# Optimization experiments

Measured on AMD Instinct MI355X. Metric: run time of the kernel, lower is better.

The kernel has to match this reference:

```python
import jax, jax.numpy as jnp
import numpy as np

B, S, N, E = 16, 2048, 256, 4096      # batch, tokens, max entities, edges per sample
H, LD, ETR = 512, 16, 768             # hidden_size, label_emb_dim, transformer dim
D = H + LD                            # graph_dim = 528
C1 = 3                                # num_edge_classes + 1
GL = 2                                # gcn_layers
NLBL = 15                             # num_node_classes + 2


def setup_inputs() -> dict:
    key = jax.random.key(0)
    ks = jax.random.split(key, 14)
    s = 0.02
    inp = {}
    inp["emb"] = jax.random.normal(ks[0], (B, S, ETR), jnp.float32)
    inp["ent_indices"] = jax.random.randint(ks[1], (B, S), 0, N + 1)
    inp["ent_labels"] = jax.random.randint(ks[2], (B, N), 0, NLBL)
    inp["edge_index"] = jax.random.randint(ks[3], (B, 2, E), 0, N + 1)
    inp["edge_attr"] = jax.random.randint(ks[4], (B, E), 0, C1)
    inp["cands"] = jax.random.randint(ks[5], (B, N + 1, N + 1), 0, 2).astype(bool)
    inp["W_red"] = jax.random.normal(ks[6], (ETR, H), jnp.float32) * s
    inp["b_red"] = jnp.zeros((H,), jnp.float32)
    inp["emb_label_tbl"] = jax.random.normal(ks[7], (NLBL, LD), jnp.float32) * s
    inp["W_gcn"] = jax.random.normal(ks[8], (C1, GL, D, D), jnp.float32) * s
    inp["b_gcn"] = jnp.zeros((C1, GL, D), jnp.float32)
    inp["W_head"] = jax.random.normal(ks[9], (D, D), jnp.float32) * s
    inp["b_head"] = jnp.zeros((D,), jnp.float32)
    inp["W_tail"] = jax.random.normal(ks[10], (D, D), jnp.float32) * s
    inp["b_tail"] = jnp.zeros((D,), jnp.float32)
    inp["W_out"] = jax.random.normal(ks[11], (D, C1), jnp.float32) * s
    inp["b_out"] = jnp.zeros((C1,), jnp.float32)
    return inp


def _gcn_layer(x, src, dst, w_e, W, b):
    """PyG GCNConv with edge weights w_e (0/1 relation mask) and self loops.
    x: [n, D]; src/dst: [E]; aggregation flow source->target."""
    n = x.shape[0]
    h = x @ W
    deg = jax.ops.segment_sum(w_e, dst, num_segments=n) + 1.0  # +1 self loop
    dinv = jax.lax.rsqrt(deg)
    coef = w_e * dinv[src] * dinv[dst]                         # D^-1/2 A D^-1/2
    agg = jax.ops.segment_sum(coef[:, None] * h[src], dst, num_segments=n)
    return agg + h / deg[:, None] + b                          # self-loop norm = 1/deg


def reference(emb, ent_indices, ent_labels, edge_index, edge_attr, cands,
              W_red, b_red, emb_label_tbl, W_gcn, b_gcn,
              W_head, b_head, W_tail, b_tail, W_out, b_out):
    n_nodes = cands.shape[1]  # max_num_ent + 1
    # fc_reduction of frozen transformer embeddings
    red = emb @ W_red + b_red                                   # [B,S,H]
    # tag-based segment aggregation: max over (mask * emb) == max(segment_max, 0)
    seg_max = jax.vmap(lambda e, ids: jax.ops.segment_max(e, ids, num_segments=n_nodes))(red, ent_indices)
    ent_hidden = jnp.maximum(seg_max, 0.0).at[:, 0, :].set(0.0)  # tag 0 stays zero
    # label embeddings: tag t uses ent_labels[:, t-1]; zeroed where label==0
    lab = emb_label_tbl[ent_labels] * (ent_labels != 0)[..., None].astype(red.dtype)
    lab0 = jnp.broadcast_to(emb_label_tbl[0], (lab.shape[0], 1, lab.shape[-1]))
    label_part = jnp.concatenate([lab0, lab], axis=1)           # [B,n_nodes,LD]
    x0 = jnp.concatenate([label_part, ent_hidden], axis=-1)     # [B,n_nodes,D]
    # multi-relation GCN: per edge class, stacked GCNConv, summed then averaged
    src, dst = edge_index[:, 0], edge_index[:, 1]
    layer_v = jax.vmap(_gcn_layer, in_axes=(0, 0, 0, 0, None, None))
    result = jnp.zeros_like(x0)
    n_cls = W_gcn.shape[0]
    for c in range(n_cls):
        w_e = (edge_attr == c).astype(x0.dtype)
        x = x0
        for l in range(W_gcn.shape[1]):
            x = layer_v(x, src, dst, w_e, W_gcn[c, l], b_gcn[c, l])
        result = result + x
    result = result / n_cls
    # head/tail projections and 'add' pairwise features gated by candidate mask
    x_head = result @ W_head + b_head
    x_tail = result @ W_tail + b_tail
    m = cands[:, :, 1:].astype(x0.dtype)                        # [B,n_nodes,n_nodes-1]
    # fc_out is linear: ((h_i + t_j) * m_ij) @ W + b == m_ij*(hW_i + tW_j) + b
    hW = x_head @ W_out                                         # [B,n_nodes,C1]
    tW = x_tail[:, 1:] @ W_out                                  # [B,n_nodes-1,C1]
    logits = (hW[:, :, None, :] + tW[:, None, :, :]) * m[..., None] + b_out
    return logits  # [B, n_nodes, n_nodes-1, C1] edge-class logits
```

## Files before the change

### kernel.cpp

```cpp
#include <hip/hip_runtime.h>
#include <hip/hip_bf16.h>

typedef unsigned short u16;
typedef __attribute__((ext_vector_type(8))) short short8;
typedef __attribute__((ext_vector_type(4))) float floatx4;

#define B_ 16
#define S_ 2048
#define NNODE 257
#define E_ 4096
#define ETR_ 768
#define H_ 512
#define D_ 528
#define KPAD 544
#define NC 3
#define NROW (B_*NNODE)
#define DD (D_*D_)

#define BM 128
#define BN 128
#define BK 32

__device__ inline u16 f2b(float x) {
    __hip_bfloat16 h = __float2bfloat16(x);
    return *(u16*)&h;
}

__device__ inline void gll16(const u16* g, u16* l) {
    __builtin_amdgcn_global_load_lds(
        (const __attribute__((address_space(1))) void*)g,
        (__attribute__((address_space(3))) void*)l,
        16, 0, 0);
}

__device__ inline int clampi(int v, int hi) { return v < hi ? v : hi; }

__global__ void cvt_bf16(const float* __restrict__ in, u16* __restrict__ out, int n4)
{
    const int i = blockIdx.x * 256 + threadIdx.x;
    if (i < n4) {
        const float4 f = ((const float4*)in)[i];
        ushort4 o;
        o.x = f2b(f.x); o.y = f2b(f.y); o.z = f2b(f.z); o.w = f2b(f.w);
        ((ushort4*)out)[i] = o;
    }
}

__global__ void transpose_cvt(const float* __restrict__ in, u16* __restrict__ out,
                              int R, int Cc, size_t instride, size_t outstride,
                              int opitch)
{
    __shared__ float t[32][33];
    const int z = blockIdx.z;
    const int tx = threadIdx.x & 31, ty = threadIdx.x >> 5;
    const int c0 = blockIdx.x * 32, r0 = blockIdx.y * 32;
    const float* ip = in + z * instride;
    u16* op = out + z * outstride;
#pragma unroll
    for (int i = 0; i < 4; i++) {
        const int r = r0 + ty + i * 8, c = c0 + tx;
        if (r < R && c < Cc) t[ty + i * 8][tx] = ip[(size_t)r * Cc + c];
    }
    __syncthreads();
#pragma unroll
    for (int i = 0; i < 4; i++) {
        const int c = c0 + ty + i * 8, r = r0 + tx;
        if (c < Cc && r < R) op[(size_t)c * opitch + r] = f2b(t[tx][ty + i * 8]);
    }
}

template<int SWZ, int OB16>
__global__ __launch_bounds__(256)
void gemm_mfma(const u16* __restrict__ A, const u16* __restrict__ Wt,
               void* __restrict__ Cv, int M, int N, int K, float scale,
               size_t astride, size_t wstride, size_t cstride)
{
    __shared__ u16 SS[8192];
    const int tid = threadIdx.x;
    const int wave = tid >> 6, lane = tid & 63;
    const int quad = lane >> 4, l16 = lane & 15;
    const int z = blockIdx.z;
    int bx = blockIdx.x, by = blockIdx.y;
    if (SWZ) {
        const int lin = blockIdx.x + (blockIdx.y << 2);
        bx = (lin >> 3) & 3;
        by = (lin & 7) + ((lin >> 5) << 3);
    }
    const int m0 = by * BM, n0 = bx * BN;

    floatx4 acc[2][8];
#pragma unroll
    for (int t = 0; t < 2; t++)
#pragma unroll
        for (int u = 0; u < 8; u++)
#pragma unroll
            for (int r = 0; r < 4; r++) acc[t][u][r] = 0.f;

    const int srow = tid >> 2;
    const int scol = (tid & 3) * 8;
    const u16* aP0 = A + z * astride + (size_t)clampi(m0 + srow,      M - 1) * K + scol;
    const u16* aP1 = A + z * astride + (size_t)clampi(m0 + 64 + srow, M - 1) * K + scol;
    const u16* bP0 = Wt + z * wstride + (size_t)clampi(n0 + srow,      N - 1) * K + scol;
    const u16* bP1 = Wt + z * wstride + (size_t)clampi(n0 + 64 + srow, N - 1) * K + scol;
    u16* const ls = &SS[0] + wave * 512;

    for (int k0 = 0; k0 < K; k0 += BK) {
        gll16(aP0 + k0, ls);
        gll16(aP1 + k0, ls + 2048);
        gll16(bP0 + k0, ls + 4096);
        gll16(bP1 + k0, ls + 6144);
        __syncthreads();
        short8 af[2], bfv[8];
        af[0] = *(const short8*)&SS[(wave * 32 + l16) * 32 + quad * 8];
        af[1] = *(const short8*)&SS[(wave * 32 + 16 + l16) * 32 + quad * 8];
#pragma unroll
        for (int u = 0; u < 8; u++)
            bfv[u] = *(const short8*)&SS[4096 + (u * 16 + l16) * 32 + quad * 8];
#pragma unroll
        for (int t = 0; t < 2; t++)
#pragma unroll
            for (int u = 0; u < 8; u++)
                acc[t][u] = __builtin_amdgcn_mfma_f32_16x16x32_bf16(af[t], bfv[u], acc[t][u], 0, 0, 0);
        __syncthreads();
    }

#pragma unroll
    for (int t = 0; t < 2; t++) {
#pragma unroll
        for (int r = 0; r < 4; r++) {
            const int m = m0 + wave * 32 + t * 16 + quad * 4 + r;
            if (m >= M) continue;
#pragma unroll
            for (int u = 0; u < 8; u++) {
                const int n = n0 + u * 16 + l16;
                if (n < N) {
                    if (OB16) {
                        u16* Cb = (u16*)Cv;
                        Cb[z * cstride + (size_t)m * N + n] = f2b(acc[t][u][r] * scale);
                    } else {
                        float* Cf = (float*)Cv;
                        Cf[z * cstride + (size_t)m * N + n] = acc[t][u][r] * scale;
                    }
                }
            }
        }
    }
}

template<int MODE>
__global__ __launch_bounds__(256)
void gemm64(const float* __restrict__ A, const float* __restrict__ W,
            const float* __restrict__ bias, float* __restrict__ C,
            int M, int N, int K, float scale,
            const int* __restrict__ segidx, float* __restrict__ segout)
{
    __shared__ float Asl[16][68];
    __shared__ float Bsl[16][64];
    const int tid = threadIdx.x;
    const int tx = tid & 15, ty = tid >> 4;
    const int m0 = blockIdx.y * 64, n0 = blockIdx.x * 64;
    const int arow = tid >> 2, acol = (tid & 3) * 4;
    const int brow = tid >> 4, bcol = (tid & 15) * 4;

    float acc[4][4];
#pragma unroll
    for (int i = 0; i < 4; i++)
#pragma unroll
        for (int j = 0; j < 4; j++) acc[i][j] = 0.f;

    for (int kk = 0; kk < K; kk += 16) {
        float4 av = make_float4(0.f, 0.f, 0.f, 0.f);
        if (m0 + arow < M) av = *(const float4*)(A + (size_t)(m0 + arow) * K + kk + acol);
        Asl[acol + 0][arow] = av.x; Asl[acol + 1][arow] = av.y;
        Asl[acol + 2][arow] = av.z; Asl[acol + 3][arow] = av.w;
        float4 bv = make_float4(0.f, 0.f, 0.f, 0.f);
        if (n0 + bcol < N) bv = *(const float4*)(W + (size_t)(kk + brow) * N + n0 + bcol);
        *(float4*)&Bsl[brow][bcol] = bv;
        __syncthreads();
#pragma unroll
        for (int k = 0; k < 16; k++) {
            const float4 a = *(const float4*)&Asl[k][ty * 4];
            const float4 b = *(const float4*)&Bsl[k][tx * 4];
            const float af[4] = { a.x, a.y, a.z, a.w };
            const float bfv[4] = { b.x, b.y, b.z, b.w };
#pragma unroll
            for (int i = 0; i < 4; i++)
#pragma unroll
                for (int j = 0; j < 4; j++) acc[i][j] += af[i] * bfv[j];
        }
        __syncthreads();
    }

#pragma unroll
    for (int i = 0; i < 4; i++) {
        const int m = m0 + ty * 4 + i;
        if (m >= M) continue;
        if (MODE == 1) {
            const int bb = m >> 11;
            const int idx = segidx[m];
            float* const srow = segout + (((size_t)bb * NNODE + idx) << 9);
#pragma unroll
            for (int j = 0; j < 4; j++) {
                const int n = n0 + tx * 4 + j;
                const float v = acc[i][j] + (bias ? bias[n] : 0.f);
                atomicMax(((int*)srow) + n, __float_as_int(v));
            }
        } else {
#pragma unroll
            for (int j = 0; j < 4; j++) {
                const int n = n0 + tx * 4 + j;
                if (n < N) {
                    const float v = acc[i][j] * scale + (bias ? bias[n] : 0.f);
                    C[(size_t)m * N + n] = v;
                }
            }
        }
    }
}

__global__ void rows_csr(const int* __restrict__ ent_indices,
                         int* __restrict__ rptr, int* __restrict__ rlist)
{
    __shared__ int cnt[NNODE];
    const int b = blockIdx.x;
    const int tid = threadIdx.x;
    const int* idx = ent_indices + (size_t)b * S_;
    for (int i = tid; i < NNODE; i += 256) cnt[i] = 0;
    __syncthreads();
    for (int r = tid; r < S_; r += 256) atomicAdd(&cnt[idx[r]], 1);
    __syncthreads();
    if (tid == 0) {
        int run = 0;
        for (int i = 0; i < NNODE; i++) { const int c = cnt[i]; cnt[i] = run; run += c; }
    }
    __syncthreads();
    for (int i = tid; i < NNODE; i += 256) rptr[b * (NNODE + 1) + i] = cnt[i];
    if (tid == 0) rptr[b * (NNODE + 1) + NNODE] = S_;
    __syncthreads();
    for (int r = tid; r < S_; r += 256) {
        const int pos = atomicAdd(&cnt[idx[r]], 1);
        rlist[(size_t)b * S_ + pos] = r;
    }
}

__global__ __launch_bounds__(256)
void segmax_x0(const u16* __restrict__ redC, const int* __restrict__ rptr,
               const int* __restrict__ rlist, const float* __restrict__ b_red,
               const int* __restrict__ ent_labels, const float* __restrict__ tbl,
               u16* __restrict__ x0b)
{
    const int bn = blockIdx.x;
    const int b = bn / NNODE, n = bn % NNODE;
    const int tid = threadIdx.x;
    const int c0 = tid * 2;
    const int start = rptr[b * (NNODE + 1) + n];
    const int end   = (n == 0) ? start : rptr[b * (NNODE + 1) + n + 1];
    float m0 = -INFINITY, m1 = -INFINITY;
    const int* rl = rlist + (size_t)b * S_;
    for (int i = start; i < end; i++) {
        const u16* row = redC + ((size_t)b * S_ + rl[i]) * H_;
        const unsigned v = *(const unsigned*)(row + c0);
        m0 = fmaxf(m0, __uint_as_float((v & 0xffffu) << 16));
        m1 = fmaxf(m1, __uint_as_float(v & 0xffff0000u));
    }
    float h0, h1;
    if (n == 0) { h0 = 0.f; h1 = 0.f; }
    else {
        h0 = fmaxf(m0 + b_red[c0], 0.f);
        h1 = fmaxf(m1 + b_red[c0 + 1], 0.f);
    }
    u16* orow = x0b + (size_t)bn * KPAD;
    *(unsigned*)(orow + 16 + c0) = (unsigned)f2b(h0) | ((unsigned)f2b(h1) << 16);
    if (tid < 16) {
        float v;
        if (n == 0) v = tbl[tid];
        else {
            const int lab = ent_labels[b * (NNODE - 1) + (n - 1)];
            v = (lab != 0) ? tbl[lab * 16 + tid] : 0.f;
        }
        orow[tid] = f2b(v);
    } else if (tid < 32) {
        orow[512 + tid] = 0;
    }
}

template<int OUTB>
__global__ void build_x0(const float* __restrict__ seg, const int* __restrict__ ent_labels,
                         const float* __restrict__ tbl, float* __restrict__ x0f,
                         u16* __restrict__ x0b)
{
    const int bn = blockIdx.x;
    const int b = bn / NNODE, n = bn % NNODE;
    const int CMAX = OUTB ? KPAD : D_;
    for (int col = threadIdx.x; col < CMAX; col += blockDim.x) {
        float v;
        if (col >= D_) {
            v = 0.f;
        } else if (col < 16) {
            if (n == 0) v = tbl[col];
            else {
                const int lab = ent_labels[b * (NNODE - 1) + (n - 1)];
                v = (lab != 0) ? tbl[lab * 16 + col] : 0.f;
            }
        } else {
            v = (n == 0) ? 0.f : seg[(((size_t)b * NNODE + n) << 9) + (col - 16)];
        }
        if (OUTB) x0b[(size_t)bn * KPAD + col] = f2b(v);
        else      x0f[(size_t)bn * D_ + col] = v;
    }
}

__global__ void csr_build(const int* __restrict__ edge_index, const int* __restrict__ edge_attr,
                          float* __restrict__ degf, int* __restrict__ csr_ptr,
                          int2* __restrict__ csr_sc)
{
    __shared__ int cnt[NC * NNODE];
    __shared__ float dinvl[NC * NNODE];
    const int b = blockIdx.x;
    const int tid = threadIdx.x;
    const int* src = edge_index + (size_t)b * 2 * E_;
    const int* dst = src + E_;
    const int* attr = edge_attr + (size_t)b * E_;

    for (int i = tid; i < NC * NNODE; i += 256) cnt[i] = 0;
    __syncthreads();
    for (int e = tid; e < E_; e += 256) atomicAdd(&cnt[attr[e] * NNODE + dst[e]], 1);
    __syncthreads();
    for (int i = tid; i < NC * NNODE; i += 256) {
        const float d = (float)cnt[i] + 1.0f;
        degf[(size_t)b * NC * NNODE + i] = d;
        dinvl[i] = rsqrtf(d);
    }
    __syncthreads();
    if (tid == 0) {
        int run = 0;
        for (int i = 0; i < NC * NNODE; i++) { const int c = cnt[i]; cnt[i] = run; run += c; }
    }
    __syncthreads();
    for (int i = tid; i < NC * NNODE; i += 256) csr_ptr[(size_t)b * NC * NNODE + i] = cnt[i];
    __syncthreads();
    for (int e = tid; e < E_; e += 256) {
        const int a = attr[e], d = dst[e], s = src[e];
        const int pos = atomicAdd(&cnt[a * NNODE + d], 1);
        const float cf = dinvl[a * NNODE + s] * dinvl[a * NNODE + d];
        csr_sc[(size_t)b * E_ + pos] = make_int2(s, __float_as_int(cf));
    }
}

template<int OUT>
__global__ __launch_bounds__(256)
void gcn_gather(const float* __restrict__ h, size_t hstride,
                const float* __restrict__ degf,
                const int* __restrict__ csr_ptr, const int2* __restrict__ csr_sc,
                const float* __restrict__ bias_base, size_t bias_stride,
                float* __restrict__ outf, u16* __restrict__ outb, size_t ostride,
                int cls0)
{
    const int bn = blockIdx.x;
    const int cls = cls0 + blockIdx.y;
    const int b = bn / NNODE, n = bn % NNODE;
    const int tid = threadIdx.x;
    const int base = b * NC * NNODE + cls * NNODE + n;
    const float d = degf[base];
    const int start = csr_ptr[base];
    const int cnt = (int)d - 1;
    const float inv = 1.0f / d;
    const float* hp = h + blockIdx.y * hstride;
    const float* bias = bias_base + cls * bias_stride;
    const float* hrow = hp + (size_t)bn * D_;
    const int c0 = tid, c1 = tid + 256, c2 = tid + 512;
    float a0 = hrow[c0] * inv + bias[c0];
    float a1 = hrow[c1] * inv + bias[c1];
    float a2 = (c2 < D_) ? hrow[c2] * inv + bias[c2] : 0.f;
    const int2* scp = csr_sc + (size_t)b * E_ + start;
    int2 sc = (cnt > 0) ? scp[0] : make_int2(0, 0);
    for (int i = 0; i < cnt; i++) {
        const int2 cur = sc;
        if (i + 1 < cnt) sc = scp[i + 1];
        const float cf = __int_as_float(cur.y);
        const float* hs = hp + ((size_t)b * NNODE + cur.x) * D_;
        a0 += cf * hs[c0];
        a1 += cf * hs[c1];
        if (c2 < D_) a2 += cf * hs[c2];
    }
    if (OUT == 0) {
        u16* orow = outb + blockIdx.y * ostride + (size_t)bn * KPAD;
        orow[c0] = f2b(a0); orow[c1] = f2b(a1); if (c2 < D_) orow[c2] = f2b(a2);
        if (tid >= 16 && tid < 32) orow[512 + tid] = 0;
    } else if (OUT == 1) {
        float* orow = outf + (size_t)bn * D_;
        orow[c0] += a0; orow[c1] += a1; if (c2 < D_) orow[c2] += a2;
    } else if (OUT == 2) {
        float* orow = outf + blockIdx.y * ostride + (size_t)bn * D_;
        orow[c0] = a0; orow[c1] = a1; if (c2 < D_) orow[c2] = a2;
    } else {
        float* orow = outf + (size_t)bn * D_;
        atomicAdd(&orow[c0], a0); atomicAdd(&orow[c1], a1);
        if (c2 < D_) atomicAdd(&orow[c2], a2);
    }
}

__global__ void rowdot3(const float* __restrict__ x, const float* __restrict__ w,
                        float* __restrict__ out)
{
    const int row = blockIdx.x;
    const int lane = threadIdx.x;
    float a0 = 0.f, a1 = 0.f, a2 = 0.f;
    for (int d = lane; d < D_; d += 64) {
        const float xv = x[(size_t)row * D_ + d];
        a0 += xv * w[d * 3 + 0];
        a1 += xv * w[d * 3 + 1];
        a2 += xv * w[d * 3 + 2];
    }
#pragma unroll
    for (int off = 32; off > 0; off >>= 1) {
        a0 += __shfl_down(a0, off, 64);
        a1 += __shfl_down(a1, off, 64);
        a2 += __shfl_down(a2, off, 64);
    }
    if (lane == 0) {
        out[(size_t)row * 3 + 0] = a0;
        out[(size_t)row * 3 + 1] = a1;
        out[(size_t)row * 3 + 2] = a2;
    }
}

__global__ void prep_heads(const float* __restrict__ W_head, const float* __restrict__ W_tail,
                           const float* __restrict__ b_head, const float* __restrict__ b_tail,
                           const float* __restrict__ W_out,
                           float* __restrict__ Whw, float* __restrict__ Wtw,
                           float* __restrict__ bias6)
{
    const int r = blockIdx.x;
    const int lane = threadIdx.x;
    const float* x; float* o;
    if (r < D_)            { x = W_head + (size_t)r * D_;        o = Whw + (size_t)r * 3; }
    else if (r < 2 * D_)   { x = W_tail + (size_t)(r - D_) * D_; o = Wtw + (size_t)(r - D_) * 3; }
    else if (r == 2 * D_)  { x = b_head;                         o = bias6; }
    else                   { x = b_tail;                         o = bias6 + 3; }
    float a0 = 0.f, a1 = 0.f, a2 = 0.f;
    for (int d = lane; d < D_; d += 64) {
        const float xv = x[d];
        a0 += xv * W_out[d * 3 + 0];
        a1 += xv * W_out[d * 3 + 1];
        a2 += xv * W_out[d * 3 + 2];
    }
#pragma unroll
    for (int off = 32; off > 0; off >>= 1) {
        a0 += __shfl_down(a0, off, 64);
        a1 += __shfl_down(a1, off, 64);
        a2 += __shfl_down(a2, off, 64);
    }
    if (lane == 0) { o[0] = a0; o[1] = a1; o[2] = a2; }
}

__global__ __launch_bounds__(256)
void rowdot6(const float* __restrict__ x3, size_t zstride,
             const float* __restrict__ Whw, const float* __restrict__ Wtw,
             const float* __restrict__ bias6,
             float* __restrict__ hw, float* __restrict__ tw)
{
    const int row = blockIdx.x * 4 + (threadIdx.x >> 6);
    const int lane = threadIdx.x & 63;
    const float* p0 = x3 + (size_t)row * D_;
    const float* p1 = p0 + zstride;
    const float* p2 = p1 + zstride;
    float h0 = 0.f, h1 = 0.f, h2 = 0.f, t0 = 0.f, t1 = 0.f, t2 = 0.f;
    for (int d = lane; d < D_; d += 64) {
        const float xv = (p0[d] + p1[d] + p2[d]) * (1.f / 3.f);
        h0 += xv * Whw[d * 3 + 0]; h1 += xv * Whw[d * 3 + 1]; h2 += xv * Whw[d * 3 + 2];
        t0 += xv * Wtw[d * 3 + 0]; t1 += xv * Wtw[d * 3 + 1]; t2 += xv * Wtw[d * 3 + 2];
    }
#pragma unroll
    for (int off = 32; off > 0; off >>= 1) {
        h0 += __shfl_down(h0, off, 64); h1 += __shfl_down(h1, off, 64); h2 += __shfl_down(h2, off, 64);
        t0 += __shfl_down(t0, off, 64); t1 += __shfl_down(t1, off, 64); t2 += __shfl_down(t2, off, 64);
    }
    if (lane == 0) {
        hw[(size_t)row * 3 + 0] = h0 + bias6[0];
        hw[(size_t)row * 3 + 1] = h1 + bias6[1];
        hw[(size_t)row * 3 + 2] = h2 + bias6[2];
        tw[(size_t)row * 3 + 0] = t0 + bias6[3];
        tw[(size_t)row * 3 + 1] = t1 + bias6[4];
        tw[(size_t)row * 3 + 2] = t2 + bias6[5];
    }
}

__global__ __launch_bounds__(256)
void final_logits(const float* __restrict__ hw, const float* __restrict__ tw,
                  const int* __restrict__ cands, const float* __restrict__ b_out,
                  float* __restrict__ out)
{
    const int bi = blockIdx.x;
    const int b = bi / NNODE;
    const int j = threadIdx.x;
    const float h0 = hw[bi * 3 + 0], h1 = hw[bi * 3 + 1], h2 = hw[bi * 3 + 2];
    const int tj = b * NNODE + 1 + j;
    const float t0 = tw[tj * 3 + 0], t1 = tw[tj * 3 + 1], t2 = tw[tj * 3 + 2];
    const float m = (cands[(size_t)bi * NNODE + 1 + j] != 0) ? 1.f : 0.f;
    const float bo0 = b_out[0], bo1 = b_out[1], bo2 = b_out[2];
    const size_t o = ((size_t)bi * 256 + j) * 3;
    out[o + 0] = (h0 + t0) * m + bo0;
    out[o + 1] = (h1 + t1) * m + bo1;
    out[o + 2] = (h2 + t2) * m + bo2;
}

extern "C" void kernel_launch(void* const* d_in, const int* in_sizes, int n_in,
                              void* d_out, int out_size, void* d_ws, size_t ws_size,
                              hipStream_t stream)
{
    const float* emb       = (const float*)d_in[0];
    const int* ent_indices = (const int*)d_in[1];
    const int* ent_labels  = (const int*)d_in[2];
    const int* edge_index  = (const int*)d_in[3];
    const int* edge_attr   = (const int*)d_in[4];
    const int* cands       = (const int*)d_in[5];
    const float* W_red     = (const float*)d_in[6];
    const float* b_red     = (const float*)d_in[7];
    const float* tbl       = (const float*)d_in[8];
    const float* W_gcn     = (const float*)d_in[9];
    const float* b_gcn     = (const float*)d_in[10];
    const float* W_head    = (const float*)d_in[11];
    const float* b_head    = (const float*)d_in[12];
    const float* W_tail    = (const float*)d_in[13];
    const float* b_tail    = (const float*)d_in[14];
    const float* W_out     = (const float*)d_in[15];
    const float* b_out     = (const float*)d_in[16];

    char* ws = (char*)d_ws;
    size_t off = 0;
    auto alloc = [&](size_t nbytes) -> char* {
        char* p = ws + off; off = (off + nbytes + 255) & ~(size_t)255; return p;
    };
    const size_t ROWB  = (size_t)NROW * D_ * sizeof(float);
    const size_t RD    = (size_t)NROW * D_;
    const size_t RD2   = (size_t)NROW * KPAD;
    const size_t WGZ   = (size_t)2 * D_ * KPAD;

    char* R0      = alloc((size_t)B_ * S_ * ETR_ * sizeof(u16));
    u16*  emb_bf  = (u16*)R0;
    float* hbuf   = (float*)R0;
    u16*  x1b     = (u16*)(R0 + 3 * ROWB);
    char* R1      = alloc((size_t)B_ * S_ * H_ * sizeof(u16));
    u16*  redC    = (u16*)R1;
    float* result3 = (float*)R1;
    int*  rptr    = (int*)alloc((size_t)B_ * (NNODE + 1) * 4);
    int*  rlist   = (int*)alloc((size_t)B_ * S_ * 4);
    u16*  x0b     = (u16*)alloc((size_t)NROW * KPAD * sizeof(u16));
    u16*  wredT   = (u16*)alloc((size_t)H_ * ETR_ * sizeof(u16));
    u16*  wgcnT   = (u16*)alloc((size_t)NC * WGZ * sizeof(u16));
    float* Whw    = (float*)alloc((size_t)D_ * 3 * 4);
    float* Wtw    = (float*)alloc((size_t)D_ * 3 * 4);
    float* bias6  = (float*)alloc(6 * 4);
    float* degf   = (float*)alloc((size_t)B_ * NC * NNODE * 4);
    float* hwp    = (float*)alloc((size_t)NROW * 3 * 4);
    float* twp    = (float*)alloc((size_t)NROW * 3 * 4);
    int* csr_ptr  = (int*)alloc((size_t)B_ * NC * NNODE * 4);
    int2* csr_sc  = (int2*)alloc((size_t)B_ * E_ * 8);
    const bool fast = (ws_size >= off);

    if (fast) {
        const int n4e = (B_ * S_ * ETR_) / 4;
        cvt_bf16<<<(n4e + 255) / 256, 256, 0, stream>>>(emb, emb_bf, n4e);
        transpose_cvt<<<dim3(16, 24, 1), 256, 0, stream>>>(W_red, wredT, ETR_, H_, 0, 0, ETR_);
        hipMemsetAsync(wgcnT, 0, (size_t)NC * WGZ * sizeof(u16), stream);
        transpose_cvt<<<dim3(17, 17, 6), 256, 0, stream>>>(W_gcn, wgcnT, D_, D_, DD, (size_t)D_ * KPAD, KPAD);

        prep_heads<<<2 * D_ + 2, 64, 0, stream>>>(W_head, W_tail, b_head, b_tail, W_out,
                                                  Whw, Wtw, bias6);

        rows_csr<<<B_, 256, 0, stream>>>(ent_indices, rptr, rlist);

        gemm_mfma<1, 1><<<dim3(H_ / BN, (B_ * S_) / BM, 1), 256, 0, stream>>>(
            emb_bf, wredT, redC, B_ * S_, H_, ETR_, 1.f, 0, 0, 0);
        segmax_x0<<<B_ * NNODE, 256, 0, stream>>>(redC, rptr, rlist, b_red,
                                                  ent_labels, tbl, x0b);

        csr_build<<<B_, 256, 0, stream>>>(edge_index, edge_attr, degf, csr_ptr, csr_sc);

        dim3 gmm((D_ + BN - 1) / BN, (NROW + BM - 1) / BM, NC);
        gemm_mfma<0, 0><<<gmm, 256, 0, stream>>>(
            x0b, wgcnT, hbuf, NROW, D_, KPAD, 1.f, 0, WGZ, RD);
        gcn_gather<0><<<dim3(NROW, NC), 256, 0, stream>>>(
            hbuf, RD, degf, csr_ptr, csr_sc, b_gcn, (size_t)2 * D_,
            nullptr, x1b, RD2, 0);
        gemm_mfma<0, 0><<<gmm, 256, 0, stream>>>(
            x1b, wgcnT + (size_t)D_ * KPAD, hbuf, NROW, D_, KPAD, 1.f, RD2, WGZ, RD);
        gcn_gather<2><<<dim3(NROW, NC), 256, 0, stream>>>(
            hbuf, RD, degf, csr_ptr, csr_sc, b_gcn + D_, (size_t)2 * D_,
            result3, nullptr, RD, 0);

        rowdot6<<<NROW / 4, 256, 0, stream>>>(result3, RD, Whw, Wtw, bias6, hwp, twp);
        final_logits<<<NROW, 256, 0, stream>>>(hwp, twp, cands, b_out, (float*)d_out);
        return;
    }

    off = 0;
    float* bufA = (float*)alloc(ROWB);
    float* bufB = (float*)alloc(ROWB);
    float* bufC = (float*)alloc(ROWB);
    float* bufD = (float*)alloc(ROWB);
    degf = (float*)alloc((size_t)B_ * NC * NNODE * 4);
    hwp  = (float*)alloc((size_t)NROW * 3 * 4);
    twp  = (float*)alloc((size_t)NROW * 3 * 4);
    csr_ptr = (int*)alloc((size_t)B_ * NC * NNODE * 4);
    csr_sc  = (int2*)alloc((size_t)B_ * E_ * 8);

    hipMemsetAsync(bufA, 0, (size_t)B_ * NNODE * H_ * 4, stream);
    hipMemsetAsync(bufD, 0, ROWB, stream);
    gemm64<1><<<dim3(H_ / 64, (B_ * S_) / 64), 256, 0, stream>>>(
        emb, W_red, b_red, nullptr, B_ * S_, H_, ETR_, 1.f, ent_indices, bufA);
    build_x0<0><<<NROW, 256, 0, stream>>>(bufA, ent_labels, tbl, bufB, nullptr);
    csr_build<<<B_, 256, 0, stream>>>(edge_index, edge_attr, degf, csr_ptr, csr_sc);
    dim3 gridG((D_ + 63) / 64, (NROW + 63) / 64);
    for (int c = 0; c < NC; c++) {
        gemm64<0><<<gridG, 256, 0, stream>>>(bufB, W_gcn + (size_t)(c * 2 + 0) * DD,
            nullptr, bufA, NROW, D_, D_, 1.f, nullptr, nullptr);
        gcn_gather<2><<<dim3(NROW, 1), 256, 0, stream>>>(bufA, 0, degf, csr_ptr, csr_sc,
            b_gcn, (size_t)2 * D_, bufC, nullptr, 0, c);
        gemm64<0><<<gridG, 256, 0, stream>>>(bufC, W_gcn + (size_t)(c * 2 + 1) * DD,
            nullptr, bufA, NROW, D_, D_, 1.f, nullptr, nullptr);
        gcn_gather<1><<<dim3(NROW, 1), 256, 0, stream>>>(bufA, 0, degf, csr_ptr, csr_sc,
            b_gcn + D_, (size_t)2 * D_, bufD, nullptr, 0, c);
    }
    gemm64<0><<<gridG, 256, 0, stream>>>(bufD, W_head, b_head, bufB,
        NROW, D_, D_, 1.f / 3.f, nullptr, nullptr);
    gemm64<0><<<gridG, 256, 0, stream>>>(bufD, W_tail, b_tail, bufC,
        NROW, D_, D_, 1.f / 3.f, nullptr, nullptr);
    rowdot3<<<NROW, 64, 0, stream>>>(bufB, W_out, hwp);
    rowdot3<<<NROW, 64, 0, stream>>>(bufC, W_out, twp);
    final_logits<<<NROW, 256, 0, stream>>>(hwp, twp, cands, b_out, (float*)d_out);
}
```

Before: 413.7 us.

## Aggregate before GCN matmul, fuse bias, and convert fp32 activations inside GEMM

The GCN layers are reordered as aggregate-then-transform (A·X then W), and the bias add moves into the GEMM epilogue. The separate emb fp32-to-bf16 conversion pass is dropped; the GEMM now loads fp32 A tiles and converts them to bf16 in registers before writing to LDS. The goal is to remove a full-size conversion kernel and one intermediate round trip. In exchange, aggregation gathers bf16 inputs and writes an fp32 buffer that the GEMM then reads. The A-tile loads lose the async global-to-LDS path and double the bytes read for A. Aggregating bf16-rounded layer-1 outputs also changes numerics slightly.

```diff
diff --git a/kernel.cpp b/kernel.cpp
--- a/kernel.cpp
+++ b/kernel.cpp
@@ -25,6 +25,9 @@
     __hip_bfloat16 h = __float2bfloat16(x);
     return *(u16*)&h;
 }
+__device__ inline float b2f(u16 u) {
+    return __uint_as_float(((unsigned)u) << 16);
+}
 
 __device__ inline void gll16(const u16* g, u16* l) {
     __builtin_amdgcn_global_load_lds(
@@ -34,17 +37,6 @@
 }
 
 __device__ inline int clampi(int v, int hi) { return v < hi ? v : hi; }
-
-__global__ void cvt_bf16(const float* __restrict__ in, u16* __restrict__ out, int n4)
-{
-    const int i = blockIdx.x * 256 + threadIdx.x;
-    if (i < n4) {
-        const float4 f = ((const float4*)in)[i];
-        ushort4 o;
-        o.x = f2b(f.x); o.y = f2b(f.y); o.z = f2b(f.z); o.w = f2b(f.w);
-        ((ushort4*)out)[i] = o;
-    }
-}
 
 __global__ void transpose_cvt(const float* __restrict__ in, u16* __restrict__ out,
                               int R, int Cc, size_t instride, size_t outstride,
@@ -71,9 +63,10 @@
 
 template<int SWZ, int OB16>
 __global__ __launch_bounds__(256)
-void gemm_mfma(const u16* __restrict__ A, const u16* __restrict__ Wt,
+void gemm_mfma(const float* __restrict__ A, const u16* __restrict__ Wt,
+               const float* __restrict__ bias_base, size_t bias_stride,
                void* __restrict__ Cv, int M, int N, int K, float scale,
-               size_t astride, size_t wstride, size_t cstride)
+               size_t astride, size_t wstride, size_t cstride, int cpitch)
 {
     __shared__ u16 SS[8192];
     const int tid = threadIdx.x;
@@ -98,17 +91,32 @@
 
     const int srow = tid >> 2;
     const int scol = (tid & 3) * 8;
-    const u16* aP0 = A + z * astride + (size_t)clampi(m0 + srow,      M - 1) * K + scol;
-    const u16* aP1 = A + z * astride + (size_t)clampi(m0 + 64 + srow, M - 1) * K + scol;
+    const float* aF0 = A + z * astride + (size_t)clampi(m0 + srow,      M - 1) * K + scol;
+    const float* aF1 = A + z * astride + (size_t)clampi(m0 + 64 + srow, M - 1) * K + scol;
     const u16* bP0 = Wt + z * wstride + (size_t)clampi(n0 + srow,      N - 1) * K + scol;
     const u16* bP1 = Wt + z * wstride + (size_t)clampi(n0 + 64 + srow, N - 1) * K + scol;
     u16* const ls = &SS[0] + wave * 512;
+    u16* const aw0 = &SS[srow * 32 + scol];
+    u16* const aw1 = &SS[2048 + srow * 32 + scol];
 
     for (int k0 = 0; k0 < K; k0 += BK) {
-        gll16(aP0 + k0, ls);
-        gll16(aP1 + k0, ls + 2048);
+        const float4 v0 = *(const float4*)(aF0 + k0);
+        const float4 v1 = *(const float4*)(aF0 + k0 + 4);
+        const float4 v2 = *(const float4*)(aF1 + k0);
+        const float4 v3 = *(const float4*)(aF1 + k0 + 4);
         gll16(bP0 + k0, ls + 4096);
         gll16(bP1 + k0, ls + 6144);
+        short8 p0, p1;
+        p0[0] = (short)f2b(v0.x); p0[1] = (short)f2b(v0.y);
+        p0[2] = (short)f2b(v0.z); p0[3] = (short)f2b(v0.w);
+        p0[4] = (short)f2b(v1.x); p0[5] = (short)f2b(v1.y);
+        p0[6] = (short)f2b(v1.z); p0[7] = (short)f2b(v1.w);
+        p1[0] = (short)f2b(v2.x); p1[1] = (short)f2b(v2.y);
+        p1[2] = (short)f2b(v2.z); p1[3] = (short)f2b(v2.w);
+        p1[4] = (short)f2b(v3.x); p1[5] = (short)f2b(v3.y);
+        p1[6] = (short)f2b(v3.z); p1[7] = (short)f2b(v3.w);
+        *(short8*)aw0 = p0;
+        *(short8*)aw1 = p1;
         __syncthreads();
         short8 af[2], bfv[8];
         af[0] = *(const short8*)&SS[(wave * 32 + l16) * 32 + quad * 8];
@@ -124,6 +132,7 @@
         __syncthreads();
     }
 
+    const float* bias = bias_base ? (bias_base + z * bias_stride) : nullptr;
 #pragma unroll
     for (int t = 0; t < 2; t++) {
 #pragma unroll
@@ -134,12 +143,13 @@
             for (int u = 0; u < 8; u++) {
                 const int n = n0 + u * 16 + l16;
                 if (n < N) {
+                    const float v = acc[t][u][r] * scale + (bias ? bias[n] : 0.f);
                     if (OB16) {
                         u16* Cb = (u16*)Cv;
-                        Cb[z * cstride + (size_t)m * N + n] = f2b(acc[t][u][r] * scale);
+                        Cb[z * cstride + (size_t)m * cpitch + n] = f2b(v);
                     } else {
                         float* Cf = (float*)Cv;
-                        Cf[z * cstride + (size_t)m * N + n] = acc[t][u][r] * scale;
+                        Cf[z * cstride + (size_t)m * cpitch + n] = v;
                     }
                 }
             }
@@ -347,6 +357,43 @@
     }
 }
 
+__global__ __launch_bounds__(256)
+void gcn_agg(const u16* __restrict__ x, size_t xzstride,
+             const float* __restrict__ degf,
+             const int* __restrict__ csr_ptr, const int2* __restrict__ csr_sc,
+             float* __restrict__ y)
+{
+    const int bn = blockIdx.x;
+    const int cls = blockIdx.y;
+    const int b = bn / NNODE, n = bn % NNODE;
+    const int tid = threadIdx.x;
+    const int base = b * NC * NNODE + cls * NNODE + n;
+    const float d = degf[base];
+    const int start = csr_ptr[base];
+    const int cnt = (int)d - 1;
+    const float inv = 1.0f / d;
+    const u16* xp = x + cls * xzstride;
+    const u16* xrow = xp + (size_t)bn * KPAD;
+    const int c0 = tid, c1 = tid + 256, c2 = tid + 512;
+    float a0 = b2f(xrow[c0]) * inv;
+    float a1 = b2f(xrow[c1]) * inv;
+    float a2 = (c2 < D_) ? b2f(xrow[c2]) * inv : 0.f;
+    const int2* scp = csr_sc + (size_t)b * E_ + start;
+    int2 sc = (cnt > 0) ? scp[0] : make_int2(0, 0);
+    for (int i = 0; i < cnt; i++) {
+        const int2 cur = sc;
+        if (i + 1 < cnt) sc = scp[i + 1];
+        const float cf = __int_as_float(cur.y);
+        const u16* xs = xp + ((size_t)b * NNODE + cur.x) * KPAD;
+        a0 += cf * b2f(xs[c0]);
+        a1 += cf * b2f(xs[c1]);
+        if (c2 < D_) a2 += cf * b2f(xs[c2]);
+    }
+    float* yr = y + ((size_t)cls * NROW + bn) * KPAD;
+    yr[c0] = a0; yr[c1] = a1;
+    if (c2 < KPAD) yr[c2] = a2;
+}
+
 template<int OUT>
 __global__ __launch_bounds__(256)
 void gcn_gather(const float* __restrict__ h, size_t hstride,
@@ -373,30 +420,20 @@
     float a1 = hrow[c1] * inv + bias[c1];
     float a2 = (c2 < D_) ? hrow[c2] * inv + bias[c2] : 0.f;
     const int2* scp = csr_sc + (size_t)b * E_ + start;
-    int2 sc = (cnt > 0) ? scp[0] : make_int2(0, 0);
     for (int i = 0; i < cnt; i++) {
-        const int2 cur = sc;
-        if (i + 1 < cnt) sc = scp[i + 1];
-        const float cf = __int_as_float(cur.y);
-        const float* hs = hp + ((size_t)b * NNODE + cur.x) * D_;
+        const int2 sc = scp[i];
+        const float cf = __int_as_float(sc.y);
+        const float* hs = hp + ((size_t)b * NNODE + sc.x) * D_;
         a0 += cf * hs[c0];
         a1 += cf * hs[c1];
         if (c2 < D_) a2 += cf * hs[c2];
     }
-    if (OUT == 0) {
-        u16* orow = outb + blockIdx.y * ostride + (size_t)bn * KPAD;
-        orow[c0] = f2b(a0); orow[c1] = f2b(a1); if (c2 < D_) orow[c2] = f2b(a2);
-        if (tid >= 16 && tid < 32) orow[512 + tid] = 0;
-    } else if (OUT == 1) {
+    if (OUT == 1) {
         float* orow = outf + (size_t)bn * D_;
         orow[c0] += a0; orow[c1] += a1; if (c2 < D_) orow[c2] += a2;
-    } else if (OUT == 2) {
-        float* orow = outf + blockIdx.y * ostride + (size_t)bn * D_;
-        orow[c0] = a0; orow[c1] = a1; if (c2 < D_) orow[c2] = a2;
     } else {
         float* orow = outf + (size_t)bn * D_;
-        atomicAdd(&orow[c0], a0); atomicAdd(&orow[c1], a1);
-        if (c2 < D_) atomicAdd(&orow[c2], a2);
+        orow[c0] = a0; orow[c1] = a1; if (c2 < D_) orow[c2] = a2;
     }
 }
 
@@ -537,10 +574,8 @@
     const size_t RD2   = (size_t)NROW * KPAD;
     const size_t WGZ   = (size_t)2 * D_ * KPAD;
 
-    char* R0      = alloc((size_t)B_ * S_ * ETR_ * sizeof(u16));
-    u16*  emb_bf  = (u16*)R0;
-    float* hbuf   = (float*)R0;
-    u16*  x1b     = (u16*)(R0 + 3 * ROWB);
+    float* ybuf   = (float*)alloc((size_t)NC * RD2 * 4);
+    u16*  x1b     = (u16*)alloc((size_t)NC * RD2 * 2);
     char* R1      = alloc((size_t)B_ * S_ * H_ * sizeof(u16));
     u16*  redC    = (u16*)R1;
     float* result3 = (float*)R1;
@@ -560,8 +595,6 @@
     const bool fast = (ws_size >= off);
 
     if (fast) {
-        const int n4e = (B_ * S_ * ETR_) / 4;
-        cvt_bf16<<<(n4e + 255) / 256, 256, 0, stream>>>(emb, emb_bf, n4e);
         transpose_cvt<<<dim3(16, 24, 1), 256, 0, stream>>>(W_red, wredT, ETR_, H_, 0, 0, ETR_);
         hipMemsetAsync(wgcnT, 0, (size_t)NC * WGZ * sizeof(u16), stream);
         transpose_cvt<<<dim3(17, 17, 6), 256, 0, stream>>>(W_gcn, wgcnT, D_, D_, DD, (size_t)D_ * KPAD, KPAD);
@@ -570,25 +603,22 @@
                                                   Whw, Wtw, bias6);
 
         rows_csr<<<B_, 256, 0, stream>>>(ent_indices, rptr, rlist);
+        csr_build<<<B_, 256, 0, stream>>>(edge_index, edge_attr, degf, csr_ptr, csr_sc);
 
         gemm_mfma<1, 1><<<dim3(H_ / BN, (B_ * S_) / BM, 1), 256, 0, stream>>>(
-            emb_bf, wredT, redC, B_ * S_, H_, ETR_, 1.f, 0, 0, 0);
+            emb, wredT, nullptr, 0, redC, B_ * S_, H_, ETR_, 1.f, 0, 0, 0, H_);
         segmax_x0<<<B_ * NNODE, 256, 0, stream>>>(redC, rptr, rlist, b_red,
                                                   ent_labels, tbl, x0b);
 
-        csr_build<<<B_, 256, 0, stream>>>(edge_index, edge_attr, degf, csr_ptr, csr_sc);
-
+        gcn_agg<<<dim3(NROW, NC), 256, 0, stream>>>(x0b, 0, degf, csr_ptr, csr_sc, ybuf);
         dim3 gmm((D_ + BN - 1) / BN, (NROW + BM - 1) / BM, NC);
+        gemm_mfma<0, 1><<<gmm, 256, 0, stream>>>(
+            ybuf, wgcnT, b_gcn, (size_t)2 * D_, x1b, NROW, D_, KPAD, 1.f,
+            RD2, WGZ, RD2, KPAD);
+        gcn_agg<<<dim3(NROW, NC), 256, 0, stream>>>(x1b, RD2, degf, csr_ptr, csr_sc, ybuf);
         gemm_mfma<0, 0><<<gmm, 256, 0, stream>>>(
-            x0b, wgcnT, hbuf, NROW, D_, KPAD, 1.f, 0, WGZ, RD);
-        gcn_gather<0><<<dim3(NROW, NC), 256, 0, stream>>>(
-            hbuf, RD, degf, csr_ptr, csr_sc, b_gcn, (size_t)2 * D_,
-            nullptr, x1b, RD2, 0);
-        gemm_mfma<0, 0><<<gmm, 256, 0, stream>>>(
-            x1b, wgcnT + (size_t)D_ * KPAD, hbuf, NROW, D_, KPAD, 1.f, RD2, WGZ, RD);
-        gcn_gather<2><<<dim3(NROW, NC), 256, 0, stream>>>(
-            hbuf, RD, degf, csr_ptr, csr_sc, b_gcn + D_, (size_t)2 * D_,
-            result3, nullptr, RD, 0);
+            ybuf, wgcnT + (size_t)D_ * KPAD, b_gcn + D_, (size_t)2 * D_,
+            result3, NROW, D_, KPAD, 1.f, RD2, WGZ, RD, D_);
 
         rowdot6<<<NROW / 4, 256, 0, stream>>>(result3, RD, Whw, Wtw, bias6, hwp, twp);
         final_logits<<<NROW, 256, 0, stream>>>(hwp, twp, cands, b_out, (float*)d_out);
```

New measurement: 450.9 us. 1.09x slower.
